# Kernel optimization log

Hardware: AMD Instinct MI355X
Metric: run time of the kernel (lower is better)

## Reference

```python
import jax, jax.numpy as jnp
import numpy as np

B, T = 16, 256
SD, AD = 24, 8
K = SD + AD           # in_dim
H = 1                 # num_heads
HD1, HD2 = 256, 256


def setup_inputs() -> dict:
    key = jax.random.key(0)
    ks = jax.random.split(key, 16)
    p = lambda kk, shp, s=0.05: jax.random.normal(kk, shp, dtype=jnp.float32) * s
    inp = {
        "state": jax.random.normal(ks[0], (B, T, SD), dtype=jnp.float32),
        "action": jax.random.normal(ks[1], (B, T, AD), dtype=jnp.float32),
        "Wq": p(ks[2], (H * K, K)), "bq": p(ks[3], (H * K,)),
        "Wk": p(ks[4], (H * K, K)), "bk": p(ks[5], (H * K,)),
        "Wv": p(ks[6], (H * K, K)), "bv": p(ks[7], (H * K,)),
        "W1": p(ks[8], (HD1, H * K + K)), "b1": p(ks[9], (HD1,)),
        "W2": p(ks[10], (HD2, HD1)), "b2": p(ks[11], (HD2,)),
        # out layer init_layer_uniform(-0.003, 0.003)
        "Wout": jax.random.uniform(ks[12], (1, HD1), minval=-0.003, maxval=0.003, dtype=jnp.float32),
        "bout": jax.random.uniform(ks[13], (1,), minval=-0.003, maxval=0.003, dtype=jnp.float32),
    }
    return inp


def reference(state, action, Wq, bq, Wk, bk, Wv, bv, W1, b1, W2, b2, Wout, bout):
    s = jnp.concatenate([state, action], axis=-1)            # (b,t,k)
    b, t, k = s.shape
    h = H
    # rel[b,i,j,:] = s[b,j] - s[b,i]
    rel = s[:, None, :, :] - s[:, :, None, :]                # (b,t,t,k)
    q = jax.nn.relu(jnp.einsum('btk,nk->btn', s, Wq) + bq).reshape(b, t, h, k)
    kk = jax.nn.relu(jnp.einsum('bijk,nk->bijn', rel, Wk) + bk).reshape(b, t, t, h, k)
    vv = jax.nn.relu(jnp.einsum('bijk,nk->bijn', rel, Wv) + bv).reshape(b, t, t, h, k)
    scores = jnp.einsum('bijhk,bihk->bhij', kk, q) / jnp.sqrt(jnp.float32(k))
    w = jax.nn.softmax(scores, axis=-1)                      # softmax over j
    x = jnp.einsum('bhij,bijhk->bihk', w, vv).reshape(b, t, h * k)
    x = jnp.concatenate([x, s], axis=-1)                     # (b,t,h*k+k)
    x = jax.nn.relu(jnp.einsum('btn,mn->btm', x, W1) + b1)
    x = jax.nn.relu(jnp.einsum('btn,mn->btm', x, W2) + b2)
    value = jnp.einsum('btn,mn->btm', x, Wout) + bout        # (b,t,1)
    return value
```

## Files before the change

### kernel.cpp

```cpp
#include <hip/hip_runtime.h>

#define NB 16
#define NT 256
#define NK 32
#define NROWS (NB * NT)
#define GQ 4
static constexpr float INV_SQRT_K = 0.17677669529663687f;

__global__ __launch_bounds__(256) void prep_kernel(
    const float* __restrict__ state, const float* __restrict__ action,
    const float* __restrict__ Wq, const float* __restrict__ bq,
    const float* __restrict__ Wk, const float* __restrict__ bk,
    const float* __restrict__ Wv, const float* __restrict__ bv,
    float* __restrict__ q, float* __restrict__ Ksb, float* __restrict__ Vsb,
    float* __restrict__ xcat)
{
    __shared__ float s_sh[8][32];
    const int tid = threadIdx.x;
    const int r = tid >> 5, n = tid & 31;
    const int row = blockIdx.x * 8 + r;
    float sval = (n < 24) ? state[row * 24 + n] : action[row * 8 + (n - 24)];
    s_sh[r][n] = sval;
    __syncthreads();
    float aq = 0.f, ak = 0.f, av = 0.f;
#pragma unroll
    for (int k = 0; k < 32; ++k) {
        float sv = s_sh[r][k];
        aq = fmaf(sv, Wq[n * 32 + k], aq);
        ak = fmaf(sv, Wk[n * 32 + k], ak);
        av = fmaf(sv, Wv[n * 32 + k], av);
    }
    q[row * 32 + n]   = fmaxf(aq + bq[n], 0.f) * INV_SQRT_K;
    Ksb[row * 32 + n] = ak + bk[n];
    Vsb[row * 32 + n] = av + bv[n];
    xcat[row * 64 + 32 + n] = sval;
}

__global__ __launch_bounds__(256) void attn_kernel(
    const float* __restrict__ q, const float* __restrict__ Ksb,
    const float* __restrict__ Vsb, const float* __restrict__ bk,
    const float* __restrict__ bv, float* __restrict__ xcat)
{
    __shared__ float Kie[GQ][32];
    __shared__ float Vie[GQ][32];
    __shared__ float qi[GQ][32];
    __shared__ float sc[GQ][256];
    __shared__ float part[GQ][8][32];
    const int tid = threadIdx.x;
    const int b  = blockIdx.x >> 6;
    const int i0 = (blockIdx.x & 63) << 2;
    const int rowbase = b * 256;

    {
        const int g = (tid >> 5) & 3, k = tid & 31;
        const int ib = (rowbase + i0 + g) * 32 + k;
        if (tid < 128) {
            Kie[g][k] = Ksb[ib] - bk[k];
            qi[g][k]  = q[ib];
        } else {
            Vie[g][k] = Vsb[ib] - bv[k];
        }
    }
    __syncthreads();

    const int j = tid;
    const float4* kp4 = (const float4*)(Ksb + (rowbase + j) * 32);
    float kr[32];
#pragma unroll
    for (int u = 0; u < 8; ++u) {
        float4 v = kp4[u];
        kr[u * 4 + 0] = v.x; kr[u * 4 + 1] = v.y;
        kr[u * 4 + 2] = v.z; kr[u * 4 + 3] = v.w;
    }
    float acc[GQ] = {0.f, 0.f, 0.f, 0.f};
#pragma unroll
    for (int k = 0; k < 32; ++k) {
        float kv = kr[k];
#pragma unroll
        for (int g = 0; g < GQ; ++g)
            acc[g] = fmaf(fmaxf(kv - Kie[g][k], 0.f), qi[g][k], acc[g]);
    }
#pragma unroll
    for (int g = 0; g < GQ; ++g) sc[g][j] = acc[g];
    __syncthreads();

    {
        const int g = tid >> 6, l = tid & 63;
        float e0 = sc[g][l], e1 = sc[g][l + 64], e2 = sc[g][l + 128], e3 = sc[g][l + 192];
        float m = fmaxf(fmaxf(e0, e1), fmaxf(e2, e3));
#pragma unroll
        for (int off = 32; off >= 1; off >>= 1) m = fmaxf(m, __shfl_xor(m, off));
        e0 = expf(e0 - m); e1 = expf(e1 - m); e2 = expf(e2 - m); e3 = expf(e3 - m);
        float ssum = ((e0 + e1) + (e2 + e3));
#pragma unroll
        for (int off = 32; off >= 1; off >>= 1) ssum += __shfl_xor(ssum, off);
        float inv = 1.f / ssum;
        sc[g][l] = e0 * inv; sc[g][l + 64] = e1 * inv;
        sc[g][l + 128] = e2 * inv; sc[g][l + 192] = e3 * inv;
    }
    __syncthreads();

    {
        const int k = tid & 31, grp = tid >> 5;
        const float* vp = Vsb + (rowbase + grp * 32) * 32;
        float vie[GQ];
#pragma unroll
        for (int g = 0; g < GQ; ++g) vie[g] = Vie[g][k];
        float xacc[GQ] = {0.f, 0.f, 0.f, 0.f};
#pragma unroll
        for (int jj = 0; jj < 32; ++jj) {
            float v = vp[jj * 32 + k];
#pragma unroll
            for (int g = 0; g < GQ; ++g)
                xacc[g] = fmaf(sc[g][grp * 32 + jj], fmaxf(v - vie[g], 0.f), xacc[g]);
        }
#pragma unroll
        for (int g = 0; g < GQ; ++g) part[g][grp][k] = xacc[g];
    }
    __syncthreads();
    if (tid < 128) {
        const int g = tid >> 5, k = tid & 31;
        float x = 0.f;
#pragma unroll
        for (int gg = 0; gg < 8; ++gg) x += part[g][gg][k];
        xcat[(rowbase + i0 + g) * 64 + k] = x;
    }
}

__global__ __launch_bounds__(256) void mlp_kernel(
    const float* __restrict__ xcat,
    const float* __restrict__ W1, const float* __restrict__ b1,
    const float* __restrict__ W2, const float* __restrict__ b2,
    const float* __restrict__ Wout, const float* __restrict__ bout,
    float* __restrict__ out)
{
    __shared__ float xc[8][64];
    __shared__ float h1[8][256];
    __shared__ float h2[8][256];
    const int tid = threadIdx.x;
    const int row0 = blockIdx.x * 8;

    ((float*)xc)[tid]       = xcat[row0 * 64 + tid];
    ((float*)xc)[tid + 256] = xcat[row0 * 64 + tid + 256];
    __syncthreads();

    const int m = tid;
    float acc[8];
#pragma unroll
    for (int r = 0; r < 8; ++r) acc[r] = 0.f;
    const float* w1p = W1 + m * 64;
#pragma unroll 8
    for (int n = 0; n < 64; ++n) {
        float w = w1p[n];
#pragma unroll
        for (int r = 0; r < 8; ++r) acc[r] = fmaf(w, xc[r][n], acc[r]);
    }
    float bb = b1[m];
#pragma unroll
    for (int r = 0; r < 8; ++r) h1[r][m] = fmaxf(acc[r] + bb, 0.f);
    __syncthreads();

#pragma unroll
    for (int r = 0; r < 8; ++r) acc[r] = 0.f;
    const float* w2p = W2 + m * 256;
#pragma unroll 4
    for (int n = 0; n < 256; ++n) {
        float w = w2p[n];
#pragma unroll
        for (int r = 0; r < 8; ++r) acc[r] = fmaf(w, h1[r][n], acc[r]);
    }
    bb = b2[m];
#pragma unroll
    for (int r = 0; r < 8; ++r) h2[r][m] = fmaxf(acc[r] + bb, 0.f);
    __syncthreads();

    if (tid < 128) {
        const int r = tid >> 4, l = tid & 15;
        float a = 0.f;
        for (int n = l; n < 256; n += 16) a = fmaf(h2[r][n], Wout[n], a);
#pragma unroll
        for (int mm = 8; mm >= 1; mm >>= 1) a += __shfl_xor(a, mm);
        if (l == 0) out[row0 + r] = a + bout[0];
    }
}

extern "C" void kernel_launch(void* const* d_in, const int* in_sizes, int n_in,
                              void* d_out, int out_size, void* d_ws, size_t ws_size,
                              hipStream_t stream)
{
    const float* state  = (const float*)d_in[0];
    const float* action = (const float*)d_in[1];
    const float* Wq     = (const float*)d_in[2];
    const float* bq     = (const float*)d_in[3];
    const float* Wk     = (const float*)d_in[4];
    const float* bk     = (const float*)d_in[5];
    const float* Wv     = (const float*)d_in[6];
    const float* bv     = (const float*)d_in[7];
    const float* W1     = (const float*)d_in[8];
    const float* b1     = (const float*)d_in[9];
    const float* W2     = (const float*)d_in[10];
    const float* b2     = (const float*)d_in[11];
    const float* Wout   = (const float*)d_in[12];
    const float* bout   = (const float*)d_in[13];
    float* out = (float*)d_out;

    float* ws   = (float*)d_ws;
    float* q    = ws;
    float* Ksb  = q   + NROWS * NK;
    float* Vsb  = Ksb + NROWS * NK;
    float* xcat = Vsb + NROWS * NK;

    prep_kernel<<<NROWS / 8, 256, 0, stream>>>(state, action, Wq, bq, Wk, bk,
                                               Wv, bv, q, Ksb, Vsb, xcat);
    attn_kernel<<<NROWS / GQ, 256, 0, stream>>>(q, Ksb, Vsb, bk, bv, xcat);
    mlp_kernel<<<NROWS / 8, 256, 0, stream>>>(xcat, W1, b1, W2, b2, Wout, bout, out);
}
```

Baseline: 122.6 us.

## Fuse attention and MLP into one kernel with eight query rows per block

Merges the attention and MLP kernels into a single kernel, so the attention output stays in shared memory instead of going through a global xcat buffer and a third launch. The query rows per block go from 4 to 8, which halves the attention grid and doubles the reuse of each K/V row load. Shared-memory reads of K, q, softmax weights and MLP activations are vectorized to float4. The cost is more shared memory and register pressure per block and half as many blocks, so fewer CUs may be kept busy.

After: 116.5 us. 5.0% less time.

```diff
diff --git a/kernel.cpp b/kernel.cpp
--- a/kernel.cpp
+++ b/kernel.cpp
@@ -1,10 +1,12 @@
 #include <hip/hip_runtime.h>
+
+typedef float f32x4 __attribute__((ext_vector_type(4)));
 
 #define NB 16
 #define NT 256
 #define NK 32
 #define NROWS (NB * NT)
-#define GQ 4
+#define GQ 8
 static constexpr float INV_SQRT_K = 0.17677669529663687f;
 
 __global__ __launch_bounds__(256) void prep_kernel(
@@ -13,7 +15,7 @@
     const float* __restrict__ Wk, const float* __restrict__ bk,
     const float* __restrict__ Wv, const float* __restrict__ bv,
     float* __restrict__ q, float* __restrict__ Ksb, float* __restrict__ Vsb,
-    float* __restrict__ xcat)
+    float* __restrict__ sbuf)
 {
     __shared__ float s_sh[8][32];
     const int tid = threadIdx.x;
@@ -30,157 +32,183 @@
         ak = fmaf(sv, Wk[n * 32 + k], ak);
         av = fmaf(sv, Wv[n * 32 + k], av);
     }
-    q[row * 32 + n]   = fmaxf(aq + bq[n], 0.f) * INV_SQRT_K;
-    Ksb[row * 32 + n] = ak + bk[n];
-    Vsb[row * 32 + n] = av + bv[n];
-    xcat[row * 64 + 32 + n] = sval;
+    q[row * 32 + n]    = fmaxf(aq + bq[n], 0.f) * INV_SQRT_K;
+    Ksb[row * 32 + n]  = ak + bk[n];
+    Vsb[row * 32 + n]  = av + bv[n];
+    sbuf[row * 32 + n] = sval;
 }
 
-__global__ __launch_bounds__(256) void attn_kernel(
+__global__ __launch_bounds__(256) void fused_kernel(
     const float* __restrict__ q, const float* __restrict__ Ksb,
     const float* __restrict__ Vsb, const float* __restrict__ bk,
-    const float* __restrict__ bv, float* __restrict__ xcat)
-{
-    __shared__ float Kie[GQ][32];
-    __shared__ float Vie[GQ][32];
-    __shared__ float qi[GQ][32];
-    __shared__ float sc[GQ][256];
-    __shared__ float part[GQ][8][32];
-    const int tid = threadIdx.x;
-    const int b  = blockIdx.x >> 6;
-    const int i0 = (blockIdx.x & 63) << 2;
-    const int rowbase = b * 256;
-
-    {
-        const int g = (tid >> 5) & 3, k = tid & 31;
-        const int ib = (rowbase + i0 + g) * 32 + k;
-        if (tid < 128) {
-            Kie[g][k] = Ksb[ib] - bk[k];
-            qi[g][k]  = q[ib];
-        } else {
-            Vie[g][k] = Vsb[ib] - bv[k];
-        }
-    }
-    __syncthreads();
-
-    const int j = tid;
-    const float4* kp4 = (const float4*)(Ksb + (rowbase + j) * 32);
-    float kr[32];
-#pragma unroll
-    for (int u = 0; u < 8; ++u) {
-        float4 v = kp4[u];
-        kr[u * 4 + 0] = v.x; kr[u * 4 + 1] = v.y;
-        kr[u * 4 + 2] = v.z; kr[u * 4 + 3] = v.w;
-    }
-    float acc[GQ] = {0.f, 0.f, 0.f, 0.f};
-#pragma unroll
-    for (int k = 0; k < 32; ++k) {
-        float kv = kr[k];
-#pragma unroll
-        for (int g = 0; g < GQ; ++g)
-            acc[g] = fmaf(fmaxf(kv - Kie[g][k], 0.f), qi[g][k], acc[g]);
-    }
-#pragma unroll
-    for (int g = 0; g < GQ; ++g) sc[g][j] = acc[g];
-    __syncthreads();
-
-    {
-        const int g = tid >> 6, l = tid & 63;
-        float e0 = sc[g][l], e1 = sc[g][l + 64], e2 = sc[g][l + 128], e3 = sc[g][l + 192];
-        float m = fmaxf(fmaxf(e0, e1), fmaxf(e2, e3));
-#pragma unroll
-        for (int off = 32; off >= 1; off >>= 1) m = fmaxf(m, __shfl_xor(m, off));
-        e0 = expf(e0 - m); e1 = expf(e1 - m); e2 = expf(e2 - m); e3 = expf(e3 - m);
-        float ssum = ((e0 + e1) + (e2 + e3));
-#pragma unroll
-        for (int off = 32; off >= 1; off >>= 1) ssum += __shfl_xor(ssum, off);
-        float inv = 1.f / ssum;
-        sc[g][l] = e0 * inv; sc[g][l + 64] = e1 * inv;
-        sc[g][l + 128] = e2 * inv; sc[g][l + 192] = e3 * inv;
-    }
-    __syncthreads();
-
-    {
-        const int k = tid & 31, grp = tid >> 5;
-        const float* vp = Vsb + (rowbase + grp * 32) * 32;
-        float vie[GQ];
-#pragma unroll
-        for (int g = 0; g < GQ; ++g) vie[g] = Vie[g][k];
-        float xacc[GQ] = {0.f, 0.f, 0.f, 0.f};
-#pragma unroll
-        for (int jj = 0; jj < 32; ++jj) {
-            float v = vp[jj * 32 + k];
-#pragma unroll
-            for (int g = 0; g < GQ; ++g)
-                xacc[g] = fmaf(sc[g][grp * 32 + jj], fmaxf(v - vie[g], 0.f), xacc[g]);
-        }
-#pragma unroll
-        for (int g = 0; g < GQ; ++g) part[g][grp][k] = xacc[g];
-    }
-    __syncthreads();
-    if (tid < 128) {
-        const int g = tid >> 5, k = tid & 31;
-        float x = 0.f;
-#pragma unroll
-        for (int gg = 0; gg < 8; ++gg) x += part[g][gg][k];
-        xcat[(rowbase + i0 + g) * 64 + k] = x;
-    }
-}
-
-__global__ __launch_bounds__(256) void mlp_kernel(
-    const float* __restrict__ xcat,
+    const float* __restrict__ bv, const float* __restrict__ sbuf,
     const float* __restrict__ W1, const float* __restrict__ b1,
     const float* __restrict__ W2, const float* __restrict__ b2,
     const float* __restrict__ Wout, const float* __restrict__ bout,
     float* __restrict__ out)
 {
-    __shared__ float xc[8][64];
-    __shared__ float h1[8][256];
-    __shared__ float h2[8][256];
+    __shared__ float Kie[GQ][32];
+    __shared__ float Vie[GQ][32];
+    __shared__ float qis[GQ][32];
+    __shared__ float sc[GQ][256];
+    __shared__ float part[GQ][8][32];
+    __shared__ float xc[GQ][64];
+    __shared__ float h1[GQ][256];
+    __shared__ float h2[GQ][256];
+
     const int tid = threadIdx.x;
-    const int row0 = blockIdx.x * 8;
-
-    ((float*)xc)[tid]       = xcat[row0 * 64 + tid];
-    ((float*)xc)[tid + 256] = xcat[row0 * 64 + tid + 256];
+    const int b  = blockIdx.x >> 5;
+    const int i0 = (blockIdx.x & 31) << 3;
+    const int rowbase = b * 256;
+    const int grow0 = rowbase + i0;
+
+    {
+        const int g = tid >> 5, k = tid & 31;
+        const int ib = (grow0 + g) * 32 + k;
+        Kie[g][k] = Ksb[ib] - bk[k];
+        qis[g][k] = q[ib];
+        Vie[g][k] = Vsb[ib] - bv[k];
+    }
+    __syncthreads();
+
+    {
+        const int j = tid;
+        const f32x4* kp4 = (const f32x4*)(Ksb + (rowbase + j) * 32);
+        f32x4 kr[8];
+#pragma unroll
+        for (int u = 0; u < 8; ++u) kr[u] = kp4[u];
+        float acc[GQ] = {};
+#pragma unroll
+        for (int k4 = 0; k4 < 8; ++k4) {
+            f32x4 kv = kr[k4];
+#pragma unroll
+            for (int g = 0; g < GQ; ++g) {
+                f32x4 ki = ((const f32x4*)Kie[g])[k4];
+                f32x4 qv = ((const f32x4*)qis[g])[k4];
+                acc[g] = fmaf(fmaxf(kv[0] - ki[0], 0.f), qv[0], acc[g]);
+                acc[g] = fmaf(fmaxf(kv[1] - ki[1], 0.f), qv[1], acc[g]);
+                acc[g] = fmaf(fmaxf(kv[2] - ki[2], 0.f), qv[2], acc[g]);
+                acc[g] = fmaf(fmaxf(kv[3] - ki[3], 0.f), qv[3], acc[g]);
+            }
+        }
+#pragma unroll
+        for (int g = 0; g < GQ; ++g) sc[g][j] = acc[g];
+    }
+    __syncthreads();
+
+    {
+        const int w = tid >> 6, l = tid & 63;
+#pragma unroll
+        for (int rr = 0; rr < 2; ++rr) {
+            const int g = w + rr * 4;
+            float e0 = sc[g][l],       e1 = sc[g][l + 64];
+            float e2 = sc[g][l + 128], e3 = sc[g][l + 192];
+            float m = fmaxf(fmaxf(e0, e1), fmaxf(e2, e3));
+#pragma unroll
+            for (int off = 32; off >= 1; off >>= 1) m = fmaxf(m, __shfl_xor(m, off));
+            e0 = expf(e0 - m); e1 = expf(e1 - m);
+            e2 = expf(e2 - m); e3 = expf(e3 - m);
+            float ssum = (e0 + e1) + (e2 + e3);
+#pragma unroll
+            for (int off = 32; off >= 1; off >>= 1) ssum += __shfl_xor(ssum, off);
+            float inv = 1.f / ssum;
+            sc[g][l] = e0 * inv;       sc[g][l + 64] = e1 * inv;
+            sc[g][l + 128] = e2 * inv; sc[g][l + 192] = e3 * inv;
+        }
+    }
+    __syncthreads();
+
+    {
+        const int k = tid & 31, grp = tid >> 5;
+        const float* vp = Vsb + (rowbase + grp * 32) * 32 + k;
+        float vie[GQ];
+#pragma unroll
+        for (int g = 0; g < GQ; ++g) vie[g] = Vie[g][k];
+        float xacc[GQ] = {};
+#pragma unroll
+        for (int jc = 0; jc < 8; ++jc) {
+            f32x4 w4[GQ];
+#pragma unroll
+            for (int g = 0; g < GQ; ++g) w4[g] = ((const f32x4*)&sc[g][grp * 32])[jc];
+#pragma unroll
+            for (int u = 0; u < 4; ++u) {
+                float v = vp[(jc * 4 + u) * 32];
+#pragma unroll
+                for (int g = 0; g < GQ; ++g)
+                    xacc[g] = fmaf(w4[g][u], fmaxf(v - vie[g], 0.f), xacc[g]);
+            }
+        }
+#pragma unroll
+        for (int g = 0; g < GQ; ++g) part[g][grp][k] = xacc[g];
+    }
+    __syncthreads();
+
+    {
+        const int g = tid >> 5, k = tid & 31;
+        float x = 0.f;
+#pragma unroll
+        for (int gg = 0; gg < 8; ++gg) x += part[g][gg][k];
+        xc[g][k] = x;
+        xc[g][32 + k] = sbuf[(grow0 + g) * 32 + k];
+    }
     __syncthreads();
 
     const int m = tid;
-    float acc[8];
-#pragma unroll
-    for (int r = 0; r < 8; ++r) acc[r] = 0.f;
-    const float* w1p = W1 + m * 64;
+    {
+        f32x4 wreg[16];
+        const f32x4* w1p4 = (const f32x4*)(W1 + m * 64);
+#pragma unroll
+        for (int u = 0; u < 16; ++u) wreg[u] = w1p4[u];
+        float acc[GQ] = {};
+#pragma unroll
+        for (int n4 = 0; n4 < 16; ++n4) {
+            f32x4 w = wreg[n4];
+#pragma unroll
+            for (int r = 0; r < GQ; ++r) {
+                f32x4 x = ((const f32x4*)xc[r])[n4];
+                acc[r] = fmaf(w[0], x[0], fmaf(w[1], x[1],
+                         fmaf(w[2], x[2], fmaf(w[3], x[3], acc[r]))));
+            }
+        }
+        float bb = b1[m];
+#pragma unroll
+        for (int r = 0; r < GQ; ++r) h1[r][m] = fmaxf(acc[r] + bb, 0.f);
+    }
+    __syncthreads();
+
+    {
+        const f32x4* w2p4 = (const f32x4*)(W2 + m * 256);
+        float acc[GQ] = {};
 #pragma unroll 8
-    for (int n = 0; n < 64; ++n) {
-        float w = w1p[n];
-#pragma unroll
-        for (int r = 0; r < 8; ++r) acc[r] = fmaf(w, xc[r][n], acc[r]);
-    }
-    float bb = b1[m];
-#pragma unroll
-    for (int r = 0; r < 8; ++r) h1[r][m] = fmaxf(acc[r] + bb, 0.f);
-    __syncthreads();
-
-#pragma unroll
-    for (int r = 0; r < 8; ++r) acc[r] = 0.f;
-    const float* w2p = W2 + m * 256;
-#pragma unroll 4
-    for (int n = 0; n < 256; ++n) {
-        float w = w2p[n];
-#pragma unroll
-        for (int r = 0; r < 8; ++r) acc[r] = fmaf(w, h1[r][n], acc[r]);
-    }
-    bb = b2[m];
-#pragma unroll
-    for (int r = 0; r < 8; ++r) h2[r][m] = fmaxf(acc[r] + bb, 0.f);
+        for (int n4 = 0; n4 < 64; ++n4) {
+            f32x4 w = w2p4[n4];
+#pragma unroll
+            for (int r = 0; r < GQ; ++r) {
+                f32x4 h = ((const f32x4*)h1[r])[n4];
+                acc[r] = fmaf(w[0], h[0], fmaf(w[1], h[1],
+                         fmaf(w[2], h[2], fmaf(w[3], h[3], acc[r]))));
+            }
+        }
+        float bb = b2[m];
+#pragma unroll
+        for (int r = 0; r < GQ; ++r) h2[r][m] = fmaxf(acc[r] + bb, 0.f);
+    }
     __syncthreads();
 
     if (tid < 128) {
         const int r = tid >> 4, l = tid & 15;
+        const f32x4* wo4 = (const f32x4*)Wout;
         float a = 0.f;
-        for (int n = l; n < 256; n += 16) a = fmaf(h2[r][n], Wout[n], a);
+#pragma unroll
+        for (int n4 = l; n4 < 64; n4 += 16) {
+            f32x4 w = wo4[n4];
+            f32x4 h = ((const f32x4*)h2[r])[n4];
+            a = fmaf(w[0], h[0], fmaf(w[1], h[1],
+                fmaf(w[2], h[2], fmaf(w[3], h[3], a))));
+        }
 #pragma unroll
         for (int mm = 8; mm >= 1; mm >>= 1) a += __shfl_xor(a, mm);
-        if (l == 0) out[row0 + r] = a + bout[0];
+        if (l == 0) out[grow0 + r] = a + bout[0];
     }
 }
 
@@ -206,12 +234,12 @@
 
     float* ws   = (float*)d_ws;
     float* q    = ws;
-    float* Ksb  = q   + NROWS * NK;
-    float* Vsb  = Ksb + NROWS * NK;
-    float* xcat = Vsb + NROWS * NK;
+    float* Ksb  = q    + NROWS * NK;
+    float* Vsb  = Ksb  + NROWS * NK;
+    float* sbuf = Vsb  + NROWS * NK;
 
     prep_kernel<<<NROWS / 8, 256, 0, stream>>>(state, action, Wq, bq, Wk, bk,
-                                               Wv, bv, q, Ksb, Vsb, xcat);
-    attn_kernel<<<NROWS / GQ, 256, 0, stream>>>(q, Ksb, Vsb, bk, bv, xcat);
-    mlp_kernel<<<NROWS / 8, 256, 0, stream>>>(xcat, W1, b1, W2, b2, Wout, bout, out);
+                                               Wv, bv, q, Ksb, Vsb, sbuf);
+    fused_kernel<<<NROWS / GQ, 256, 0, stream>>>(q, Ksb, Vsb, bk, bv, sbuf,
+                                                 W1, b1, W2, b2, Wout, bout, out);
 }
```
